# Kernel optimization log

Hardware: AMD Instinct MI355X
Metric: run time of the kernel (lower is better)

Reference implementation:

```python
import jax, jax.numpy as jnp
import numpy as np

HEAD_SIZE = 64


def setup_inputs() -> dict:
    key = jax.random.key(0)
    kx, kk, kq, kv = jax.random.split(key, 4)
    B, T, C = 4, 4096, 1024
    x = jax.random.normal(kx, (B, T, C), dtype=jnp.float32)
    Wk = jax.random.normal(kk, (C, HEAD_SIZE), dtype=jnp.float32) * 0.02
    Wq = jax.random.normal(kq, (C, HEAD_SIZE), dtype=jnp.float32) * 0.02
    Wv = jax.random.normal(kv, (C, HEAD_SIZE), dtype=jnp.float32) * 0.02
    return {"x": x, "Wk": Wk, "Wq": Wq, "Wv": Wv}


def reference(x, Wk, Wq, Wv):
    # x: (B,T,C); projections to (B,T,H)
    T = x.shape[1]
    k = jnp.einsum('btc,ch->bth', x, Wk)
    q = jnp.einsum('btc,ch->bth', x, Wq)
    v = jnp.einsum('btc,ch->bth', x, Wv)
    scale = 1.0 / jnp.sqrt(jnp.float32(HEAD_SIZE))
    wei = jnp.einsum('bth,bsh->bts', q, k) * scale  # (B,T,T)
    causal = jnp.tril(jnp.ones((T, T), dtype=bool))
    wei = jnp.where(causal, wei, -jnp.inf)
    wei = jax.nn.softmax(wei, axis=-1)
    out = jnp.einsum('bts,bsh->bth', wei, v)  # (B,T,H)
    return out
```

## Files before the change

kernel.cpp:

```cpp
#include <hip/hip_runtime.h>

typedef __attribute__((ext_vector_type(8))) short short8;
typedef __attribute__((ext_vector_type(4))) float f32x4;
typedef unsigned short u16;

#define BB 4
#define TT 4096
#define CC 1024
#define HH 64

static __device__ __forceinline__ u16 f2bf(float f) {
    unsigned int u = __float_as_uint(f);
    unsigned int r = (u + 0x7FFFu + ((u >> 16) & 1u)) >> 16;
    return (u16)r;
}

static __device__ __forceinline__ int swz(int row, int chunk) {
    return row * 64 + ((chunk ^ (row & 7)) << 3);
}

__global__ void detect_dtype(const u16* __restrict__ xu, int* __restrict__ flag) {
    int lane = threadIdx.x;
    int cnt = 0;
    for (int i = lane; i < 1024; i += 64) {
        u16 u = xu[2 * i];
        int e = (u >> 7) & 0xFF;
        cnt += (e >= 100 && e <= 140) ? 1 : 0;
    }
    for (int d = 1; d < 64; d <<= 1) cnt += __shfl_xor(cnt, d);
    if (lane == 0) *flag = (cnt > 512) ? 1 : 0;
}

__global__ void wt_transpose(const void* __restrict__ Wk, const void* __restrict__ Wq,
                             const void* __restrict__ Wv, u16* __restrict__ Wtp,
                             const int* __restrict__ flag) {
    const int isbf = *flag;
    int r = blockIdx.x;
    int p = r >> 6;
    int n = r & 63;
    int nt = n >> 4, nl = n & 15;
    const void* W = (p == 0) ? Wq : (p == 1) ? Wk : Wv;
    int k0 = threadIdx.x * 4;
    int kb = k0 >> 6, k2 = (k0 >> 5) & 1, quad = (k0 >> 3) & 3, half = (k0 >> 2) & 1;
    ushort4 v;
    if (isbf) {
        const u16* Wb = (const u16*)W;
        v.x = Wb[(k0 + 0) * HH + n]; v.y = Wb[(k0 + 1) * HH + n];
        v.z = Wb[(k0 + 2) * HH + n]; v.w = Wb[(k0 + 3) * HH + n];
    } else {
        const float* Wf = (const float*)W;
        v.x = f2bf(Wf[(k0 + 0) * HH + n]); v.y = f2bf(Wf[(k0 + 1) * HH + n]);
        v.z = f2bf(Wf[(k0 + 2) * HH + n]); v.w = f2bf(Wf[(k0 + 3) * HH + n]);
    }
    size_t off16 = ((size_t)((p * 4 + nt) * 16 + kb) * 2 + k2) * 64 + quad * 16 + nl;
    *reinterpret_cast<ushort4*>(Wtp + off16 * 8 + half * 4) = v;
}

__global__ __launch_bounds__(256) void qkv_proj(const void* __restrict__ x,
                                                const u16* __restrict__ Wtp,
                                                u16* __restrict__ qo, u16* __restrict__ ko,
                                                u16* __restrict__ vo, const int* __restrict__ flag) {
    __shared__ __align__(16) u16 xs[16 * 1024];
    __shared__ __align__(16) u16 tls[4][3][256];
    const int isbf = *flag;
    const int tid = threadIdx.x;
    const int lane = tid & 63;
    const int w = tid >> 6;
    const int l15 = lane & 15;
    const int quad = lane >> 4;
    int phys = blockIdx.x;
    int rb = (phys & 7) * 128 + (phys >> 3);
    const int g0r = rb * 16;

    #pragma unroll
    for (int j = 0; j < 8; j++) {
        int c = tid + j * 256;
        int row = c >> 7, ck = c & 127;
        int dst = row * 1024 + ((ck ^ (row & 7)) << 3);
        if (isbf) {
            uint4 d = *reinterpret_cast<const uint4*>((const u16*)x + (size_t)(g0r + row) * CC + ck * 8);
            *reinterpret_cast<uint4*>(xs + dst) = d;
        } else {
            const float4* pf = reinterpret_cast<const float4*>((const float*)x + (size_t)(g0r + row) * CC + ck * 8);
            float4 a0 = pf[0], a1 = pf[1];
            ushort4 lo; lo.x = f2bf(a0.x); lo.y = f2bf(a0.y); lo.z = f2bf(a0.z); lo.w = f2bf(a0.w);
            ushort4 hi; hi.x = f2bf(a1.x); hi.y = f2bf(a1.y); hi.z = f2bf(a1.z); hi.w = f2bf(a1.w);
            *reinterpret_cast<ushort4*>(xs + dst) = lo;
            *reinterpret_cast<ushort4*>(xs + dst + 4) = hi;
        }
    }
    __syncthreads();

    f32x4 zero = {0.f, 0.f, 0.f, 0.f};
    f32x4 acc[3];
    #pragma unroll
    for (int i = 0; i < 3; i++) acc[i] = zero;

    for (int kb = 0; kb < 16; kb++) {
        #pragma unroll
        for (int k2 = 0; k2 < 2; k2++) {
            int ck = kb * 8 + k2 * 4 + quad;
            short8 af = *reinterpret_cast<const short8*>(xs + l15 * 1024 + ((ck ^ (l15 & 7)) << 3));
            #pragma unroll
            for (int p = 0; p < 3; p++) {
                short8 bf = *reinterpret_cast<const short8*>(
                    Wtp + ((((size_t)(p * 4 + w) * 16 + kb) * 2 + k2) * 64 + lane) * 8);
                acc[p] = __builtin_amdgcn_mfma_f32_16x16x32_bf16(af, bf, acc[p], 0, 0, 0);
            }
        }
    }

    const float qscale = 0.18033688011112042f;
    #pragma unroll
    for (int p = 0; p < 3; p++) {
        if (p < 2) {
            float sc = (p == 0) ? qscale : 1.f;
            #pragma unroll
            for (int r = 0; r < 4; r++)
                tls[w][p][(quad * 4 + r) * 16 + l15] = f2bf(acc[p][r] * sc);
        } else {
            #pragma unroll
            for (int r = 0; r < 4; r++)
                tls[w][p][l15 * 16 + quad * 4 + r] = f2bf(acc[p][r]);
        }
    }
    #pragma unroll
    for (int p = 0; p < 2; p++) {
        int t = lane >> 2, seg = lane & 3;
        ushort4 d = *reinterpret_cast<const ushort4*>(&tls[w][p][t * 16 + seg * 4]);
        u16* dst = (p == 0) ? qo : ko;
        *reinterpret_cast<ushort4*>(dst + (size_t)(g0r + t) * HH + w * 16 + seg * 4) = d;
    }
    {
        int c = lane >> 2, seg = lane & 3;
        ushort4 d = *reinterpret_cast<const ushort4*>(&tls[w][2][c * 16 + seg * 4]);
        int b = rb >> 8;
        int kt = (g0r & 4095) >> 6;
        int toff = g0r & 63;
        *reinterpret_cast<ushort4*>(vo + ((size_t)((b * 64 + kt) * 64 + w * 16 + c)) * 64 + toff + seg * 4) = d;
    }
}

__global__ __launch_bounds__(256) void attn(const u16* __restrict__ qp, const u16* __restrict__ kp,
                                            const u16* __restrict__ vp, float* __restrict__ acco,
                                            float* __restrict__ accl, void* __restrict__ outv,
                                            const int* __restrict__ flag, int nsplit) {
    __shared__ __align__(16) u16 kst[64 * 64];
    __shared__ __align__(16) u16 vts[64 * 64];
    __shared__ __align__(16) u16 pb[4][16 * 64];
    const int isbf = *flag;
    const int tid = threadIdx.x;
    const int lane = tid & 63;
    const int w = tid >> 6;
    const int l15 = lane & 15;
    const int quad = lane >> 4;

    int u = blockIdx.x;
    int b, qt, ks;
    if (nsplit == 1) {
        b = u >> 6;
        int raw = u & 63;
        qt = (raw & 1) ? (63 - (raw >> 1)) : (raw >> 1);
        ks = 0;
    } else {
        int per = 64 * nsplit;
        b = u / per;
        int rem = u - b * per;
        qt = rem / nsplit;
        ks = rem - qt * nsplit;
    }
    int qbase = qt * 64;
    int diag = qt;
    int nkt = diag + 1;
    if (ks >= nkt) return;

    short8 aq[2];
    {
        const u16* qrow = qp + (size_t)(b * TT + qbase + w * 16 + l15) * HH;
        aq[0] = *reinterpret_cast<const short8*>(qrow + quad * 8);
        aq[1] = *reinterpret_cast<const short8*>(qrow + 32 + quad * 8);
    }

    f32x4 zero = {0.f, 0.f, 0.f, 0.f};
    f32x4 o[4];
    #pragma unroll
    for (int i = 0; i < 4; i++) o[i] = zero;
    f32x4 lsum = zero;

    for (int kt = ks; kt < nkt; kt += nsplit) {
        __syncthreads();
        #pragma unroll
        for (int j = 0; j < 2; j++) {
            int cc = tid + j * 256;
            int row = cc >> 3, c8 = cc & 7;
            int dst = swz(row, c8);
            uint4 dk = *reinterpret_cast<const uint4*>(kp + (size_t)(b * TT + kt * 64) * HH + cc * 8);
            *reinterpret_cast<uint4*>(&kst[dst]) = dk;
            uint4 dv = *reinterpret_cast<const uint4*>(vp + ((size_t)(b * 64 + kt)) * 64 * 64 + cc * 8);
            *reinterpret_cast<uint4*>(&vts[dst]) = dv;
        }
        __syncthreads();
        f32x4 s[4];
        #pragma unroll
        for (int i = 0; i < 4; i++) s[i] = zero;
        #pragma unroll
        for (int k2 = 0; k2 < 2; k2++) {
            #pragma unroll
            for (int nt = 0; nt < 4; nt++) {
                short8 bf = *reinterpret_cast<const short8*>(&kst[swz(nt * 16 + l15, k2 * 4 + quad)]);
                s[nt] = __builtin_amdgcn_mfma_f32_16x16x32_bf16(aq[k2], bf, s[nt], 0, 0, 0);
            }
        }
        const int rg = qbase + w * 16 + quad * 4;
        const bool dm = (kt == diag);
        #pragma unroll
        for (int nt = 0; nt < 4; nt++) {
            int key = kt * 64 + nt * 16 + l15;
            #pragma unroll
            for (int r = 0; r < 4; r++) {
                float p = __builtin_amdgcn_exp2f(s[nt][r]);
                if (dm && key > rg + r) p = 0.f;
                s[nt][r] = p;
            }
        }
        #pragma unroll
        for (int nt = 0; nt < 4; nt++) lsum = lsum + s[nt];
        #pragma unroll
        for (int nt = 0; nt < 4; nt++) {
            int chunk = nt * 2 + (l15 >> 3);
            int off = l15 & 7;
            #pragma unroll
            for (int r = 0; r < 4; r++) {
                int row = quad * 4 + r;
                pb[w][row * 64 + ((chunk ^ (row & 7)) << 3) + off] = f2bf(s[nt][r]);
            }
        }
        #pragma unroll
        for (int k2 = 0; k2 < 2; k2++) {
            short8 ap = *reinterpret_cast<const short8*>(&pb[w][swz(l15, k2 * 4 + quad)]);
            #pragma unroll
            for (int nt = 0; nt < 4; nt++) {
                short8 bv = *reinterpret_cast<const short8*>(&vts[swz(nt * 16 + l15, k2 * 4 + quad)]);
                o[nt] = __builtin_amdgcn_mfma_f32_16x16x32_bf16(ap, bv, o[nt], 0, 0, 0);
            }
        }
    }

    #pragma unroll
    for (int d = 1; d < 16; d <<= 1) {
        f32x4 t;
        #pragma unroll
        for (int r = 0; r < 4; r++) t[r] = __shfl_xor(lsum[r], d);
        lsum = lsum + t;
    }
    const int g0 = b * TT + qbase + w * 16 + quad * 4;

    if (nsplit == 1) {
        f32x4 inv;
        #pragma unroll
        for (int r = 0; r < 4; r++) inv[r] = 1.0f / lsum[r];
        if (isbf) {
            u16* outp = (u16*)outv;
            #pragma unroll
            for (int nt = 0; nt < 4; nt++)
                #pragma unroll
                for (int r = 0; r < 4; r++)
                    outp[(size_t)(g0 + r) * HH + nt * 16 + l15] = f2bf(o[nt][r] * inv[r]);
        } else {
            float* outp = (float*)outv;
            #pragma unroll
            for (int nt = 0; nt < 4; nt++)
                #pragma unroll
                for (int r = 0; r < 4; r++)
                    outp[(size_t)(g0 + r) * HH + nt * 16 + l15] = o[nt][r] * inv[r];
        }
    } else {
        float* accos = acco + (size_t)ks * (BB * TT * HH);
        float* accls = accl + (size_t)ks * (BB * TT);
        #pragma unroll
        for (int nt = 0; nt < 4; nt++)
            #pragma unroll
            for (int r = 0; r < 4; r++)
                accos[(size_t)(g0 + r) * HH + nt * 16 + l15] = o[nt][r];
        if (l15 == 0) {
            #pragma unroll
            for (int r = 0; r < 4; r++) accls[g0 + r] = lsum[r];
        }
    }
}

__global__ __launch_bounds__(256) void attn_finalize(const float* __restrict__ acco,
                                                     const float* __restrict__ accl,
                                                     void* __restrict__ outv,
                                                     const int* __restrict__ flag, int nsplit) {
    const int isbf = *flag;
    int i = blockIdx.x * blockDim.x + threadIdx.x;
    int row = i >> 4;
    int qt = (row & (TT - 1)) >> 6;
    int nact = min(nsplit, qt + 1);
    float4 ov = reinterpret_cast<const float4*>(acco)[i];
    float l = accl[row];
    for (int s = 1; s < nact; s++) {
        float4 t = reinterpret_cast<const float4*>(acco + (size_t)s * (BB * TT * HH))[i];
        ov.x += t.x; ov.y += t.y; ov.z += t.z; ov.w += t.w;
        l += accl[(size_t)s * (BB * TT) + row];
    }
    float inv = 1.0f / l;
    if (isbf) {
        ushort4 s;
        s.x = f2bf(ov.x * inv); s.y = f2bf(ov.y * inv);
        s.z = f2bf(ov.z * inv); s.w = f2bf(ov.w * inv);
        reinterpret_cast<ushort4*>(outv)[i] = s;
    } else {
        float4 s = {ov.x * inv, ov.y * inv, ov.z * inv, ov.w * inv};
        reinterpret_cast<float4*>(outv)[i] = s;
    }
}

extern "C" void kernel_launch(void* const* d_in, const int* in_sizes, int n_in,
                              void* d_out, int out_size, void* d_ws, size_t ws_size,
                              hipStream_t stream) {
    const void* x  = d_in[0];
    const void* Wk = d_in[1];
    const void* Wq = d_in[2];
    const void* Wv = d_in[3];
    char* ws = (char*)d_ws;
    u16* qo = (u16*)(ws);
    u16* ko = (u16*)(ws + (size_t)2 * 1024 * 1024);
    u16* vo = (u16*)(ws + (size_t)4 * 1024 * 1024);
    u16* Wtp = (u16*)(ws + (size_t)6 * 1024 * 1024);
    int* flag = (int*)(ws + (size_t)6 * 1024 * 1024 + 768 * 1024);
    float* acco = (float*)(ws + (size_t)7 * 1024 * 1024);
    float* accl = (float*)(ws + (size_t)23 * 1024 * 1024);

    const size_t need_split = (size_t)24 * 1024 * 1024;
    const int nsplit = (ws_size >= need_split) ? 4 : 1;

    detect_dtype<<<1, 64, 0, stream>>>((const u16*)x, flag);
    wt_transpose<<<192, 256, 0, stream>>>(Wk, Wq, Wv, Wtp, flag);
    qkv_proj<<<1024, 256, 0, stream>>>(x, Wtp, qo, ko, vo, flag);
    if (nsplit > 1) {
        attn<<<BB * 64 * nsplit, 256, 0, stream>>>(qo, ko, vo, acco, accl, d_out, flag, nsplit);
        attn_finalize<<<(BB * TT * HH / 4) / 256, 256, 0, stream>>>(acco, accl, d_out, flag, nsplit);
    } else {
        attn<<<BB * 64, 256, 0, stream>>>(qo, ko, vo, acco, accl, d_out, flag, 1);
    }
}
```

Before: 156.8 us.

## Prefetch K/V tiles into registers, raise split to 8, reverse tile order

The K and V tiles for the next split iteration are now loaded into registers while the current tile is being computed, so global-load latency overlaps with the MFMA work. MFMA sections are wrapped in s_setprio hints. The split-K factor goes from 4 to 8, with the workspace layout for the partial accumulators enlarged to match, and query tiles are scheduled heaviest-first. The aim is better latency hiding and load balance, at the cost of more registers, more partial-sum traffic in finalize, and needing a larger workspace for the split path to run.

```diff
diff --git a/kernel.cpp b/kernel.cpp
--- a/kernel.cpp
+++ b/kernel.cpp
@@ -166,8 +166,9 @@
         int per = 64 * nsplit;
         b = u / per;
         int rem = u - b * per;
-        qt = rem / nsplit;
-        ks = rem - qt * nsplit;
+        int i = rem / nsplit;
+        qt = 63 - i;
+        ks = rem - i * nsplit;
     }
     int qbase = qt * 64;
     int diag = qt;
@@ -181,28 +182,41 @@
         aq[1] = *reinterpret_cast<const short8*>(qrow + 32 + quad * 8);
     }
 
+    const int cc0 = tid, cc1 = tid + 256;
+    const int dst0 = swz(cc0 >> 3, cc0 & 7);
+    const int dst1 = swz(cc1 >> 3, cc1 & 7);
+    const u16* kbase = kp + (size_t)b * TT * HH;
+    const u16* vbase = vp + (size_t)b * 64 * 64 * 64;
+
     f32x4 zero = {0.f, 0.f, 0.f, 0.f};
     f32x4 o[4];
     #pragma unroll
     for (int i = 0; i < 4; i++) o[i] = zero;
     f32x4 lsum = zero;
 
+    uint4 rk0 = *reinterpret_cast<const uint4*>(kbase + (size_t)ks * 4096 + cc0 * 8);
+    uint4 rk1 = *reinterpret_cast<const uint4*>(kbase + (size_t)ks * 4096 + cc1 * 8);
+    uint4 rv0 = *reinterpret_cast<const uint4*>(vbase + (size_t)ks * 4096 + cc0 * 8);
+    uint4 rv1 = *reinterpret_cast<const uint4*>(vbase + (size_t)ks * 4096 + cc1 * 8);
+
     for (int kt = ks; kt < nkt; kt += nsplit) {
         __syncthreads();
-        #pragma unroll
-        for (int j = 0; j < 2; j++) {
-            int cc = tid + j * 256;
-            int row = cc >> 3, c8 = cc & 7;
-            int dst = swz(row, c8);
-            uint4 dk = *reinterpret_cast<const uint4*>(kp + (size_t)(b * TT + kt * 64) * HH + cc * 8);
-            *reinterpret_cast<uint4*>(&kst[dst]) = dk;
-            uint4 dv = *reinterpret_cast<const uint4*>(vp + ((size_t)(b * 64 + kt)) * 64 * 64 + cc * 8);
-            *reinterpret_cast<uint4*>(&vts[dst]) = dv;
-        }
+        *reinterpret_cast<uint4*>(&kst[dst0]) = rk0;
+        *reinterpret_cast<uint4*>(&kst[dst1]) = rk1;
+        *reinterpret_cast<uint4*>(&vts[dst0]) = rv0;
+        *reinterpret_cast<uint4*>(&vts[dst1]) = rv1;
         __syncthreads();
+        int ktn = kt + nsplit;
+        if (ktn < nkt) {
+            rk0 = *reinterpret_cast<const uint4*>(kbase + (size_t)ktn * 4096 + cc0 * 8);
+            rk1 = *reinterpret_cast<const uint4*>(kbase + (size_t)ktn * 4096 + cc1 * 8);
+            rv0 = *reinterpret_cast<const uint4*>(vbase + (size_t)ktn * 4096 + cc0 * 8);
+            rv1 = *reinterpret_cast<const uint4*>(vbase + (size_t)ktn * 4096 + cc1 * 8);
+        }
         f32x4 s[4];
         #pragma unroll
         for (int i = 0; i < 4; i++) s[i] = zero;
+        __builtin_amdgcn_s_setprio(1);
         #pragma unroll
         for (int k2 = 0; k2 < 2; k2++) {
             #pragma unroll
@@ -211,6 +225,7 @@
                 s[nt] = __builtin_amdgcn_mfma_f32_16x16x32_bf16(aq[k2], bf, s[nt], 0, 0, 0);
             }
         }
+        __builtin_amdgcn_s_setprio(0);
         const int rg = qbase + w * 16 + quad * 4;
         const bool dm = (kt == diag);
         #pragma unroll
@@ -235,6 +250,7 @@
                 pb[w][row * 64 + ((chunk ^ (row & 7)) << 3) + off] = f2bf(s[nt][r]);
             }
         }
+        __builtin_amdgcn_s_setprio(1);
         #pragma unroll
         for (int k2 = 0; k2 < 2; k2++) {
             short8 ap = *reinterpret_cast<const short8*>(&pb[w][swz(l15, k2 * 4 + quad)]);
@@ -244,6 +260,7 @@
                 o[nt] = __builtin_amdgcn_mfma_f32_16x16x32_bf16(ap, bv, o[nt], 0, 0, 0);
             }
         }
+        __builtin_amdgcn_s_setprio(0);
     }
 
     #pragma unroll
@@ -331,10 +348,10 @@
     u16* Wtp = (u16*)(ws + (size_t)6 * 1024 * 1024);
     int* flag = (int*)(ws + (size_t)6 * 1024 * 1024 + 768 * 1024);
     float* acco = (float*)(ws + (size_t)7 * 1024 * 1024);
-    float* accl = (float*)(ws + (size_t)23 * 1024 * 1024);
-
-    const size_t need_split = (size_t)24 * 1024 * 1024;
-    const int nsplit = (ws_size >= need_split) ? 4 : 1;
+    float* accl = (float*)(ws + (size_t)39 * 1024 * 1024);
+
+    const size_t need_split = (size_t)40 * 1024 * 1024;
+    const int nsplit = (ws_size >= need_split) ? 8 : 1;
 
     detect_dtype<<<1, 64, 0, stream>>>((const u16*)x, flag);
     wt_transpose<<<192, 256, 0, stream>>>(Wk, Wq, Wv, Wtp, flag);
```

Result: faster. 146.2 us (-6.8%).
